# Kernel optimization log

Measured on AMD Instinct MI355X. Metric: run time of the kernel, lower is better.

## Reference

```python
import jax, jax.numpy as jnp
import numpy as np

D_MODEL = 1024
NHEAD = 16
HEAD_DIM = D_MODEL // NHEAD
ROPE_BASE = 10000.0


def rope_cos_sin(seq_len, dim, dtype=jnp.float32):
    inv_freq = 1.0 / (ROPE_BASE ** (jnp.arange(0, dim, 2, dtype=jnp.float32) / dim))
    t = jnp.arange(seq_len, dtype=jnp.float32)
    freqs = jnp.einsum('i,j->ij', t, inv_freq)        # [S, dim/2]
    emb = jnp.concatenate([freqs, freqs], axis=-1)    # [S, dim]
    return emb.astype(dtype), jnp.cos(emb).astype(dtype), jnp.sin(emb).astype(dtype)


def rotate_half(x):
    x1, x2 = jnp.split(x, 2, axis=-1)
    return jnp.concatenate([-x2, x1], axis=-1)


def setup_inputs() -> dict:
    key = jax.random.key(0)
    ks = jax.random.split(key, 11)
    B, S, D = 2, 2048, D_MODEL
    std = 1.0 / np.sqrt(D)
    return {
        'query': jax.random.normal(ks[0], (B, S, D), jnp.float32),
        'key_': jax.random.normal(ks[1], (B, S, D), jnp.float32),
        'value': jax.random.normal(ks[2], (B, S, D), jnp.float32),
        'Wq': jax.random.uniform(ks[3], (D, D), jnp.float32, -std, std),
        'bq': jax.random.uniform(ks[4], (D,), jnp.float32, -std, std),
        'Wk': jax.random.uniform(ks[5], (D, D), jnp.float32, -std, std),
        'bk': jax.random.uniform(ks[6], (D,), jnp.float32, -std, std),
        'Wv': jax.random.uniform(ks[7], (D, D), jnp.float32, -std, std),
        'bv': jax.random.uniform(ks[8], (D,), jnp.float32, -std, std),
        'Wo': jax.random.uniform(ks[9], (D, D), jnp.float32, -std, std),
        'bo': jax.random.uniform(ks[10], (D,), jnp.float32, -std, std),
    }


def reference(query, key_, value, Wq, bq, Wk, bk, Wv, bv, Wo, bo):
    B, T, D = query.shape
    S = key_.shape[1]
    H, Hd = NHEAD, HEAD_DIM
    scale = Hd ** -0.5
    # projections (torch Linear: x @ W^T + b), reshape to [B, H, L, Hd]
    q = (query @ Wq.T + bq).reshape(B, T, H, Hd).transpose(0, 2, 1, 3)
    k = (key_ @ Wk.T + bk).reshape(B, S, H, Hd).transpose(0, 2, 1, 3)
    v = (value @ Wv.T + bv).reshape(B, S, H, Hd).transpose(0, 2, 1, 3)
    # RoPE
    _, cos, sin = rope_cos_sin(max(T, S), Hd, query.dtype)
    cos_q, sin_q = cos[:T][None, None], sin[:S][None, None]
    q = q * cos_q + rotate_half(q) * sin_q
    k = k * cos_q + rotate_half(k) * sin_q
    # attention
    scores = jnp.einsum('bhtd,bhsd->bhts', q, k) * scale
    attn = jax.nn.softmax(scores, axis=-1)
    out = jnp.einsum('bhts,bhsd->bhtd', attn, v)
    out = out.transpose(0, 2, 1, 3).reshape(B, T, D)
    return out @ Wo.T + bo
```

## Files before the change

### kernel.cpp

```cpp
#include <hip/hip_runtime.h>
#include <hip/hip_bf16.h>
#include <math.h>

using bf16x8 = __attribute__((ext_vector_type(8))) short;
using f32x4  = __attribute__((ext_vector_type(4))) float;

#define MFMA16(a,b,c) __builtin_amdgcn_mfma_f32_16x16x32_bf16(a,b,c,0,0,0)

static __device__ __forceinline__ short f2bf(float f) {
    __hip_bfloat16 h = __float2bfloat16(f);
    return *reinterpret_cast<short*>(&h);
}

__global__ void prep_cast(const float* q, const float* k, const float* v,
                          const float* wq, const float* wk, const float* wv, const float* wo,
                          short* xq, short* xk, short* xv,
                          short* bwq, short* bwk, short* bwv, short* bwo) {
    const long NBIG = 1L << 20;
    const long NW   = 1L << 18;
    const long total = 3*NBIG + 4*NW;
    for (long i = (long)blockIdx.x*blockDim.x + threadIdx.x; i < total; i += (long)gridDim.x*blockDim.x) {
        const float* src; short* dst; long j = i;
        if (j < NBIG)              { src = q;  dst = xq;  }
        else if ((j -= NBIG) < NBIG) { src = k;  dst = xk;  }
        else if ((j -= NBIG) < NBIG) { src = v;  dst = xv;  }
        else if ((j -= NBIG) < NW)   { src = wq; dst = bwq; }
        else if ((j -= NW) < NW)     { src = wk; dst = bwk; }
        else if ((j -= NW) < NW)     { src = wv; dst = bwv; }
        else { j -= NW;              src = wo; dst = bwo; }
        float4 f = reinterpret_cast<const float4*>(src)[j];
        ushort4 o;
        o.x = (ushort)f2bf(f.x); o.y = (ushort)f2bf(f.y);
        o.z = (ushort)f2bf(f.z); o.w = (ushort)f2bf(f.w);
        reinterpret_cast<ushort4*>(dst)[j] = o;
    }
}

__global__ void rope_table(float* cost, float* sint) {
    int i = blockIdx.x*blockDim.x + threadIdx.x;
    int s = i >> 5, j = i & 31;
    double inv = pow(10000.0, -(double)j / 32.0);
    double a = (double)s * inv;
    cost[i] = (float)cos(a);
    sint[i] = (float)sin(a);
}

__device__ __forceinline__ void gemm_tile(const short* A, const short* B,
                                          int brow, int bcol, f32x4 (&acc)[4][4]) {
    __shared__ __align__(16) short Al[128*32];
    __shared__ __align__(16) short Bl[128*32];
    const int t = threadIdx.x;
    const int l = t & 63, qi = l & 15, h = l >> 4;
    const int w = t >> 6, wr = w >> 1, wc = w & 1;
    const f32x4 z4 = {0.f, 0.f, 0.f, 0.f};
#pragma unroll
    for (int i = 0; i < 4; ++i)
#pragma unroll
        for (int j = 0; j < 4; ++j) acc[i][j] = z4;

    for (int kt = 0; kt < 32; ++kt) {
        __syncthreads();
#pragma unroll
        for (int cc = 0; cc < 2; ++cc) {
            int c = t + (cc << 8);
            int row = c >> 2, off = (c & 3) << 3;
            int4 va = *(const int4*)(A + (long)(brow + row)*1024 + (kt << 5) + off);
            int4 vb = *(const int4*)(B + (long)(bcol + row)*1024 + (kt << 5) + off);
            *(int4*)(Al + (c << 3)) = va;
            *(int4*)(Bl + (c << 3)) = vb;
        }
        __syncthreads();
        bf16x8 af[4], bfr[4];
#pragma unroll
        for (int mf = 0; mf < 4; ++mf)
            af[mf] = *(const bf16x8*)(Al + (wr*64 + mf*16 + qi)*32 + h*8);
#pragma unroll
        for (int nf = 0; nf < 4; ++nf)
            bfr[nf] = *(const bf16x8*)(Bl + (wc*64 + nf*16 + qi)*32 + h*8);
#pragma unroll
        for (int mf = 0; mf < 4; ++mf)
#pragma unroll
            for (int nf = 0; nf < 4; ++nf)
                acc[mf][nf] = MFMA16(af[mf], bfr[nf], acc[mf][nf]);
    }
}

__global__ __launch_bounds__(256, 2)
void gemm_qkv_kernel(const short* xq, const short* xk, const short* xv,
                     const short* wq, const short* wk, const short* wv,
                     const float* biq, const float* bik, const float* biv,
                     short* qo, short* ko, short* vo,
                     const float* cost, const float* sint) {
    const int mode = blockIdx.z;
    const short* A    = mode == 0 ? xq  : (mode == 1 ? xk  : xv);
    const short* B    = mode == 0 ? wq  : (mode == 1 ? wk  : wv);
    const float* bias = mode == 0 ? biq : (mode == 1 ? bik : biv);
    const int brow = blockIdx.x * 128, bcol = blockIdx.y * 128;
    f32x4 acc[4][4];
    gemm_tile(A, B, brow, bcol, acc);

    const int t = threadIdx.x;
    const int l = t & 63, qi = l & 15, h = l >> 4;
    const int w = t >> 6, wr = w >> 1, wc = w & 1;
    const int n0 = bcol + wc*64, m0 = brow + wr*64;

    if (mode < 2) {
        short* dst = mode == 0 ? qo : ko;
        const float sc = (mode == 0) ? 0.125f : 1.0f;
#pragma unroll
        for (int nf = 0; nf < 2; ++nf) {
            const int j = nf*16 + qi;
            const float b0 = bias[n0 + nf*16 + qi];
            const float b1 = bias[n0 + (nf+2)*16 + qi];
#pragma unroll
            for (int mf = 0; mf < 4; ++mf) {
#pragma unroll
                for (int r = 0; r < 4; ++r) {
                    int m = m0 + mf*16 + 4*h + r;
                    int s = m & 2047;
                    float c  = cost[s*32 + j];
                    float si = sint[s*32 + j];
                    float x0 = acc[mf][nf  ][r] + b0;
                    float x1 = acc[mf][nf+2][r] + b1;
                    dst[(long)m*1024 + n0 + nf*16 + qi]      = f2bf((x0*c - x1*si) * sc);
                    dst[(long)m*1024 + n0 + (nf+2)*16 + qi]  = f2bf((x1*c + x0*si) * sc);
                }
            }
        }
    } else {
#pragma unroll
        for (int mf = 0; mf < 4; ++mf) {
#pragma unroll
            for (int nf = 0; nf < 4; ++nf) {
                int col = n0 + nf*16 + qi;
                float bb = bias[col];
                int mbase = m0 + mf*16 + 4*h;
                int bb_  = mbase >> 11, s0 = mbase & 2047;
                int hh = col >> 6, d = col & 63;
                ushort4 pk;
                pk.x = (ushort)f2bf(acc[mf][nf][0] + bb);
                pk.y = (ushort)f2bf(acc[mf][nf][1] + bb);
                pk.z = (ushort)f2bf(acc[mf][nf][2] + bb);
                pk.w = (ushort)f2bf(acc[mf][nf][3] + bb);
                *(ushort4*)(vo + (long)((bb_*16 + hh)*64 + d)*2048 + s0) = pk;
            }
        }
    }
}

__global__ __launch_bounds__(256, 2)
void gemm_o_kernel(const short* A, const short* B, const float* bias, float* out) {
    const int brow = blockIdx.x * 128, bcol = blockIdx.y * 128;
    f32x4 acc[4][4];
    gemm_tile(A, B, brow, bcol, acc);
    const int t = threadIdx.x;
    const int l = t & 63, qi = l & 15, h = l >> 4;
    const int w = t >> 6, wr = w >> 1, wc = w & 1;
    const int n0 = bcol + wc*64, m0 = brow + wr*64;
#pragma unroll
    for (int nf = 0; nf < 4; ++nf) {
        float bb = bias[n0 + nf*16 + qi];
#pragma unroll
        for (int mf = 0; mf < 4; ++mf) {
#pragma unroll
            for (int r = 0; r < 4; ++r) {
                int m = m0 + mf*16 + 4*h + r;
                out[(long)m*1024 + n0 + nf*16 + qi] = acc[mf][nf][r] + bb;
            }
        }
    }
}

__global__ __launch_bounds__(256, 2)
void attn_kernel(const short* qw, const short* kw, const short* vtw, short* ow) {
    __shared__ __align__(16) short Kl[64*64];
    __shared__ __align__(16) short Vl[64*64];
    __shared__ __align__(16) short Pl[4][32*64];
    const int t = threadIdx.x;
    const int w = t >> 6, l = t & 63, qi = l & 15, h = l >> 4;
    const int b = blockIdx.z, hh = blockIdx.y;
    const long qrow0 = (long)b*2048 + blockIdx.x*128 + w*32;
    short* myP = &Pl[w][0];

    bf16x8 bqf[2][2];
#pragma unroll
    for (int nf = 0; nf < 2; ++nf)
#pragma unroll
        for (int kf = 0; kf < 2; ++kf)
            bqf[nf][kf] = *(const bf16x8*)(qw + (qrow0 + nf*16 + qi)*1024 + hh*64 + kf*32 + h*8);

    const f32x4 z4 = {0.f, 0.f, 0.f, 0.f};
    f32x4 o[2][4];
#pragma unroll
    for (int mi = 0; mi < 2; ++mi)
#pragma unroll
        for (int nd = 0; nd < 4; ++nd) o[mi][nd] = z4;
    float mrun[2] = {-INFINITY, -INFINITY};
    float lrun[2] = {0.f, 0.f};

    const short* Kg = kw  + (long)b*2048*1024 + hh*64;
    const short* Vg = vtw + (long)(b*16 + hh)*64*2048;

    for (int jt = 0; jt < 32; ++jt) {
        __syncthreads();
#pragma unroll
        for (int cc = 0; cc < 2; ++cc) {
            int c  = t + (cc << 8);
            int r0 = c >> 3, e0 = (c & 7) << 3;
            int4 kv = *(const int4*)(Kg + (long)(jt*64 + r0)*1024 + e0);
            int4 vv = *(const int4*)(Vg + (long)r0*2048 + jt*64 + e0);
            *(int4*)((char*)Kl + (((r0*64 + e0)*2) ^ ((r0 & 7) << 4))) = kv;
            *(int4*)((char*)Vl + (((r0*64 + e0)*2) ^ ((r0 & 7) << 4))) = vv;
        }
        __syncthreads();

        f32x4 sc[4][2];
#pragma unroll
        for (int mf = 0; mf < 4; ++mf) { sc[mf][0] = z4; sc[mf][1] = z4; }
#pragma unroll
        for (int kf = 0; kf < 2; ++kf) {
#pragma unroll
            for (int mf = 0; mf < 4; ++mf) {
                bf16x8 ka = *(const bf16x8*)((char*)Kl +
                    ((((mf*16 + qi)*64 + kf*32 + h*8)*2) ^ ((qi & 7) << 4)));
                sc[mf][0] = MFMA16(ka, bqf[0][kf], sc[mf][0]);
                sc[mf][1] = MFMA16(ka, bqf[1][kf], sc[mf][1]);
            }
        }

        float csc[2];
#pragma unroll
        for (int nf = 0; nf < 2; ++nf) {
            float tm = -INFINITY;
#pragma unroll
            for (int mf = 0; mf < 4; ++mf)
#pragma unroll
                for (int r = 0; r < 4; ++r) tm = fmaxf(tm, sc[mf][nf][r]);
            tm = fmaxf(tm, __shfl_xor(tm, 16));
            tm = fmaxf(tm, __shfl_xor(tm, 32));
            float mnew = fmaxf(mrun[nf], tm);
            float corr = __expf(mrun[nf] - mnew);
            float ts = 0.f;
#pragma unroll
            for (int mf = 0; mf < 4; ++mf) {
                float p0 = __expf(sc[mf][nf][0] - mnew);
                float p1 = __expf(sc[mf][nf][1] - mnew);
                float p2 = __expf(sc[mf][nf][2] - mnew);
                float p3 = __expf(sc[mf][nf][3] - mnew);
                ts += p0 + p1 + p2 + p3;
                ushort4 pk;
                pk.x = (ushort)f2bf(p0); pk.y = (ushort)f2bf(p1);
                pk.z = (ushort)f2bf(p2); pk.w = (ushort)f2bf(p3);
                *(ushort4*)((char*)myP +
                    ((((nf*16 + qi)*64 + mf*16 + 4*h)*2) ^ ((qi & 7) << 4))) = pk;
            }
            ts += __shfl_xor(ts, 16);
            ts += __shfl_xor(ts, 32);
            lrun[nf] = lrun[nf]*corr + ts;
            mrun[nf] = mnew;
            csc[nf] = corr;
        }

#pragma unroll
        for (int mi = 0; mi < 2; ++mi)
#pragma unroll
            for (int r = 0; r < 4; ++r) {
                float f = __shfl(csc[mi], 4*h + r);
#pragma unroll
                for (int nd = 0; nd < 4; ++nd) o[mi][nd][r] *= f;
            }

#pragma unroll
        for (int kf = 0; kf < 2; ++kf) {
            bf16x8 pa[2], vb[4];
#pragma unroll
            for (int mi = 0; mi < 2; ++mi)
                pa[mi] = *(const bf16x8*)((char*)myP +
                    ((((mi*16 + qi)*64 + kf*32 + h*8)*2) ^ ((qi & 7) << 4)));
#pragma unroll
            for (int nd = 0; nd < 4; ++nd)
                vb[nd] = *(const bf16x8*)((char*)Vl +
                    ((((nd*16 + qi)*64 + kf*32 + h*8)*2) ^ ((qi & 7) << 4)));
#pragma unroll
            for (int mi = 0; mi < 2; ++mi)
#pragma unroll
                for (int nd = 0; nd < 4; ++nd)
                    o[mi][nd] = MFMA16(pa[mi], vb[nd], o[mi][nd]);
        }
    }

    float rinv[2] = {1.f/lrun[0], 1.f/lrun[1]};
#pragma unroll
    for (int mi = 0; mi < 2; ++mi)
#pragma unroll
        for (int r = 0; r < 4; ++r) {
            float f = __shfl(rinv[mi], 4*h + r);
#pragma unroll
            for (int nd = 0; nd < 4; ++nd)
                ow[(qrow0 + mi*16 + 4*h + r)*1024 + hh*64 + nd*16 + qi] =
                    f2bf(o[mi][nd][r] * f);
        }
}

extern "C" void kernel_launch(void* const* d_in, const int* in_sizes, int n_in,
                              void* d_out, int out_size, void* d_ws, size_t ws_size,
                              hipStream_t stream) {
    const float* query = (const float*)d_in[0];
    const float* key_  = (const float*)d_in[1];
    const float* value = (const float*)d_in[2];
    const float* Wq = (const float*)d_in[3];
    const float* bq = (const float*)d_in[4];
    const float* Wk = (const float*)d_in[5];
    const float* bk = (const float*)d_in[6];
    const float* Wv = (const float*)d_in[7];
    const float* bv = (const float*)d_in[8];
    const float* Wo = (const float*)d_in[9];
    const float* bo = (const float*)d_in[10];
    float* out = (float*)d_out;

    char* ws = (char*)d_ws;
    const size_t MB = 1u << 20;
    short* xq  = (short*)(ws);
    short* xk  = (short*)(ws + 8*MB);
    short* xv  = (short*)(ws + 16*MB);
    short* wqb = (short*)(ws + 24*MB);
    short* wkb = (short*)(ws + 26*MB);
    short* wvb = (short*)(ws + 28*MB);
    short* wob = (short*)(ws + 30*MB);
    short* qws = (short*)(ws + 32*MB);
    short* kws = (short*)(ws + 40*MB);
    short* vtw = (short*)(ws + 48*MB);
    float* cost = (float*)(ws + 56*MB);
    float* sint = (float*)(ws + 56*MB + 2048*32*4);
    short* attn = xq;

    hipLaunchKernelGGL(prep_cast, dim3(2048), dim3(256), 0, stream,
                       query, key_, value, Wq, Wk, Wv, Wo,
                       xq, xk, xv, wqb, wkb, wvb, wob);
    hipLaunchKernelGGL(rope_table, dim3(256), dim3(256), 0, stream, cost, sint);
    hipLaunchKernelGGL(gemm_qkv_kernel, dim3(32, 8, 3), dim3(256), 0, stream,
                       xq, xk, xv, wqb, wkb, wvb, bq, bk, bv,
                       qws, kws, vtw, cost, sint);
    hipLaunchKernelGGL(attn_kernel, dim3(16, 16, 2), dim3(256), 0, stream,
                       qws, kws, vtw, attn);
    hipLaunchKernelGGL(gemm_o_kernel, dim3(32, 8), dim3(256), 0, stream,
                       attn, wob, bo, out);
}
```

Before: 250.5 us.

## Double-buffer K/V tiles in attention and use direct global-to-LDS loads in GEMM

The attention kernel now double-buffers its K/V shared-memory tiles. It issues the global loads for the next tile into registers before the current tile's MFMAs, writes them to the other buffer afterward, and drops one barrier per iteration. It also raises wave priority around the MFMA blocks with s_setprio. The GEMM tile loader switches to the global_load_lds builtin, so data goes straight from global memory into LDS without a register round trip. The double buffer doubles K/V LDS use, which may affect occupancy at two blocks per CU, and the direct-to-LDS path relies on the per-wave layout matching the fragment reads.

Result: slower. 268.2 us (+7.0%).

```diff
diff --git a/kernel.cpp b/kernel.cpp
--- a/kernel.cpp
+++ b/kernel.cpp
@@ -6,6 +6,10 @@
 using f32x4  = __attribute__((ext_vector_type(4))) float;
 
 #define MFMA16(a,b,c) __builtin_amdgcn_mfma_f32_16x16x32_bf16(a,b,c,0,0,0)
+
+#define GLOAD_LDS16(g, s) __builtin_amdgcn_global_load_lds( \
+    (const __attribute__((address_space(1))) unsigned int*)(const void*)(g), \
+    (__attribute__((address_space(3))) unsigned int*)(void*)(s), 16, 0, 0)
 
 static __device__ __forceinline__ short f2bf(float f) {
     __hip_bfloat16 h = __float2bfloat16(f);
@@ -58,17 +62,19 @@
 #pragma unroll
         for (int j = 0; j < 4; ++j) acc[i][j] = z4;
 
+    const int srow = w*32 + (l >> 2);
+    const int scol = (l & 3) << 3;
+    const short* ga = A + (long)(brow + srow)*1024 + scol;
+    const short* gb = B + (long)(bcol + srow)*1024 + scol;
+    short* la = Al + w*32*32;
+    short* lb = Bl + w*32*32;
+
     for (int kt = 0; kt < 32; ++kt) {
         __syncthreads();
-#pragma unroll
-        for (int cc = 0; cc < 2; ++cc) {
-            int c = t + (cc << 8);
-            int row = c >> 2, off = (c & 3) << 3;
-            int4 va = *(const int4*)(A + (long)(brow + row)*1024 + (kt << 5) + off);
-            int4 vb = *(const int4*)(B + (long)(bcol + row)*1024 + (kt << 5) + off);
-            *(int4*)(Al + (c << 3)) = va;
-            *(int4*)(Bl + (c << 3)) = vb;
-        }
+        GLOAD_LDS16(ga + (kt << 5),            la);
+        GLOAD_LDS16(ga + (kt << 5) + 16*1024,  la + 16*32);
+        GLOAD_LDS16(gb + (kt << 5),            lb);
+        GLOAD_LDS16(gb + (kt << 5) + 16*1024,  lb + 16*32);
         __syncthreads();
         bf16x8 af[4], bfr[4];
 #pragma unroll
@@ -173,8 +179,8 @@
 
 __global__ __launch_bounds__(256, 2)
 void attn_kernel(const short* qw, const short* kw, const short* vtw, short* ow) {
-    __shared__ __align__(16) short Kl[64*64];
-    __shared__ __align__(16) short Vl[64*64];
+    __shared__ __align__(16) short Kl[2][64*64];
+    __shared__ __align__(16) short Vl[2][64*64];
     __shared__ __align__(16) short Pl[4][32*64];
     const int t = threadIdx.x;
     const int w = t >> 6, l = t & 63, qi = l & 15, h = l >> 4;
@@ -201,32 +207,47 @@
     const short* Kg = kw  + (long)b*2048*1024 + hh*64;
     const short* Vg = vtw + (long)(b*16 + hh)*64*2048;
 
+    const int c0 = t, c1 = t + 256;
+    const int r0a = c0 >> 3, e0a = (c0 & 7) << 3;
+    const int r0b = c1 >> 3, e0b = (c1 & 7) << 3;
+    int4 kreg[2], vreg[2];
+
+    kreg[0] = *(const int4*)(Kg + (long)r0a*1024 + e0a);
+    vreg[0] = *(const int4*)(Vg + (long)r0a*2048 + e0a);
+    kreg[1] = *(const int4*)(Kg + (long)r0b*1024 + e0b);
+    vreg[1] = *(const int4*)(Vg + (long)r0b*2048 + e0b);
+    *(int4*)((char*)Kl[0] + (((r0a*64 + e0a)*2) ^ ((r0a & 7) << 4))) = kreg[0];
+    *(int4*)((char*)Vl[0] + (((r0a*64 + e0a)*2) ^ ((r0a & 7) << 4))) = vreg[0];
+    *(int4*)((char*)Kl[1 & 0] + (((r0b*64 + e0b)*2) ^ ((r0b & 7) << 4))) = kreg[1];
+    *(int4*)((char*)Vl[0] + (((r0b*64 + e0b)*2) ^ ((r0b & 7) << 4))) = vreg[1];
+
+    int cur = 0;
     for (int jt = 0; jt < 32; ++jt) {
         __syncthreads();
-#pragma unroll
-        for (int cc = 0; cc < 2; ++cc) {
-            int c  = t + (cc << 8);
-            int r0 = c >> 3, e0 = (c & 7) << 3;
-            int4 kv = *(const int4*)(Kg + (long)(jt*64 + r0)*1024 + e0);
-            int4 vv = *(const int4*)(Vg + (long)r0*2048 + jt*64 + e0);
-            *(int4*)((char*)Kl + (((r0*64 + e0)*2) ^ ((r0 & 7) << 4))) = kv;
-            *(int4*)((char*)Vl + (((r0*64 + e0)*2) ^ ((r0 & 7) << 4))) = vv;
-        }
-        __syncthreads();
+        if (jt < 31) {
+            kreg[0] = *(const int4*)(Kg + (long)((jt+1)*64 + r0a)*1024 + e0a);
+            vreg[0] = *(const int4*)(Vg + (long)r0a*2048 + (jt+1)*64 + e0a);
+            kreg[1] = *(const int4*)(Kg + (long)((jt+1)*64 + r0b)*1024 + e0b);
+            vreg[1] = *(const int4*)(Vg + (long)r0b*2048 + (jt+1)*64 + e0b);
+        }
+        const short* Kc = Kl[cur];
+        const short* Vc = Vl[cur];
 
         f32x4 sc[4][2];
 #pragma unroll
         for (int mf = 0; mf < 4; ++mf) { sc[mf][0] = z4; sc[mf][1] = z4; }
+        __builtin_amdgcn_s_setprio(1);
 #pragma unroll
         for (int kf = 0; kf < 2; ++kf) {
 #pragma unroll
             for (int mf = 0; mf < 4; ++mf) {
-                bf16x8 ka = *(const bf16x8*)((char*)Kl +
+                bf16x8 ka = *(const bf16x8*)((const char*)Kc +
                     ((((mf*16 + qi)*64 + kf*32 + h*8)*2) ^ ((qi & 7) << 4)));
                 sc[mf][0] = MFMA16(ka, bqf[0][kf], sc[mf][0]);
                 sc[mf][1] = MFMA16(ka, bqf[1][kf], sc[mf][1]);
             }
         }
+        __builtin_amdgcn_s_setprio(0);
 
         float csc[2];
 #pragma unroll
@@ -270,6 +291,7 @@
                 for (int nd = 0; nd < 4; ++nd) o[mi][nd][r] *= f;
             }
 
+        __builtin_amdgcn_s_setprio(1);
 #pragma unroll
         for (int kf = 0; kf < 2; ++kf) {
             bf16x8 pa[2], vb[4];
@@ -279,7 +301,7 @@
                     ((((mi*16 + qi)*64 + kf*32 + h*8)*2) ^ ((qi & 7) << 4)));
 #pragma unroll
             for (int nd = 0; nd < 4; ++nd)
-                vb[nd] = *(const bf16x8*)((char*)Vl +
+                vb[nd] = *(const bf16x8*)((const char*)Vc +
                     ((((nd*16 + qi)*64 + kf*32 + h*8)*2) ^ ((qi & 7) << 4)));
 #pragma unroll
             for (int mi = 0; mi < 2; ++mi)
@@ -287,6 +309,16 @@
                 for (int nd = 0; nd < 4; ++nd)
                     o[mi][nd] = MFMA16(pa[mi], vb[nd], o[mi][nd]);
         }
+        __builtin_amdgcn_s_setprio(0);
+
+        if (jt < 31) {
+            int nb = cur ^ 1;
+            *(int4*)((char*)Kl[nb] + (((r0a*64 + e0a)*2) ^ ((r0a & 7) << 4))) = kreg[0];
+            *(int4*)((char*)Vl[nb] + (((r0a*64 + e0a)*2) ^ ((r0a & 7) << 4))) = vreg[0];
+            *(int4*)((char*)Kl[nb] + (((r0b*64 + e0b)*2) ^ ((r0b & 7) << 4))) = kreg[1];
+            *(int4*)((char*)Vl[nb] + (((r0b*64 + e0b)*2) ^ ((r0b & 7) << 4))) = vreg[1];
+        }
+        cur ^= 1;
     }
 
     float rinv[2] = {1.f/lrun[0], 1.f/lrun[1]};
```

## Double-buffer GEMM tiles with direct global-to-LDS loads and MFMA priority hints

Applied to the files above, without the earlier changes.

The shared GEMM tile loop now uses two LDS buffers filled by global_load_lds, so the next K-slice streams into shared memory while MFMAs run on the current one, with one barrier per iteration instead of two. The GEMM kernels' launch bounds go from 2 to 3 blocks per CU. s_setprio brackets are added around the MFMA sections in both the GEMMs and the attention kernel. Shared memory per GEMM block doubles, which may limit the higher occupancy target, and the tighter launch bound may force register spills.

Result: no change. 246.3 us (-1.7%).

```diff
diff --git a/kernel.cpp b/kernel.cpp
--- a/kernel.cpp
+++ b/kernel.cpp
@@ -6,6 +6,10 @@
 using f32x4  = __attribute__((ext_vector_type(4))) float;
 
 #define MFMA16(a,b,c) __builtin_amdgcn_mfma_f32_16x16x32_bf16(a,b,c,0,0,0)
+
+#define GLOAD_LDS16(g, s) __builtin_amdgcn_global_load_lds( \
+    (const __attribute__((address_space(1))) unsigned int*)(const void*)(g), \
+    (__attribute__((address_space(3))) unsigned int*)(void*)(s), 16, 0, 0)
 
 static __device__ __forceinline__ short f2bf(float f) {
     __hip_bfloat16 h = __float2bfloat16(f);
@@ -47,8 +51,8 @@
 
 __device__ __forceinline__ void gemm_tile(const short* A, const short* B,
                                           int brow, int bcol, f32x4 (&acc)[4][4]) {
-    __shared__ __align__(16) short Al[128*32];
-    __shared__ __align__(16) short Bl[128*32];
+    __shared__ __align__(16) short Al[2][128*32];
+    __shared__ __align__(16) short Bl[2][128*32];
     const int t = threadIdx.x;
     const int l = t & 63, qi = l & 15, h = l >> 4;
     const int w = t >> 6, wr = w >> 1, wc = w & 1;
@@ -58,34 +62,49 @@
 #pragma unroll
         for (int j = 0; j < 4; ++j) acc[i][j] = z4;
 
+    const int srow = w*32 + (l >> 2);
+    const int scol = (l & 3) << 3;
+    const short* ga = A + (long)(brow + srow)*1024 + scol;
+    const short* gb = B + (long)(bcol + srow)*1024 + scol;
+    const int lo = w*32*32;
+
+    GLOAD_LDS16(ga,            Al[0] + lo);
+    GLOAD_LDS16(ga + 16*1024,  Al[0] + lo + 16*32);
+    GLOAD_LDS16(gb,            Bl[0] + lo);
+    GLOAD_LDS16(gb + 16*1024,  Bl[0] + lo + 16*32);
+    asm volatile("s_waitcnt vmcnt(0)");
+    __syncthreads();
+
+    int cur = 0;
     for (int kt = 0; kt < 32; ++kt) {
-        __syncthreads();
-#pragma unroll
-        for (int cc = 0; cc < 2; ++cc) {
-            int c = t + (cc << 8);
-            int row = c >> 2, off = (c & 3) << 3;
-            int4 va = *(const int4*)(A + (long)(brow + row)*1024 + (kt << 5) + off);
-            int4 vb = *(const int4*)(B + (long)(bcol + row)*1024 + (kt << 5) + off);
-            *(int4*)(Al + (c << 3)) = va;
-            *(int4*)(Bl + (c << 3)) = vb;
-        }
-        __syncthreads();
+        if (kt < 31) {
+            int nb = cur ^ 1;
+            GLOAD_LDS16(ga + ((kt+1) << 5),            Al[nb] + lo);
+            GLOAD_LDS16(ga + ((kt+1) << 5) + 16*1024,  Al[nb] + lo + 16*32);
+            GLOAD_LDS16(gb + ((kt+1) << 5),            Bl[nb] + lo);
+            GLOAD_LDS16(gb + ((kt+1) << 5) + 16*1024,  Bl[nb] + lo + 16*32);
+        }
         bf16x8 af[4], bfr[4];
 #pragma unroll
         for (int mf = 0; mf < 4; ++mf)
-            af[mf] = *(const bf16x8*)(Al + (wr*64 + mf*16 + qi)*32 + h*8);
+            af[mf] = *(const bf16x8*)(Al[cur] + (wr*64 + mf*16 + qi)*32 + h*8);
 #pragma unroll
         for (int nf = 0; nf < 4; ++nf)
-            bfr[nf] = *(const bf16x8*)(Bl + (wc*64 + nf*16 + qi)*32 + h*8);
+            bfr[nf] = *(const bf16x8*)(Bl[cur] + (wc*64 + nf*16 + qi)*32 + h*8);
+        __builtin_amdgcn_s_setprio(1);
 #pragma unroll
         for (int mf = 0; mf < 4; ++mf)
 #pragma unroll
             for (int nf = 0; nf < 4; ++nf)
                 acc[mf][nf] = MFMA16(af[mf], bfr[nf], acc[mf][nf]);
-    }
-}
-
-__global__ __launch_bounds__(256, 2)
+        __builtin_amdgcn_s_setprio(0);
+        asm volatile("s_waitcnt vmcnt(0)");
+        __syncthreads();
+        cur ^= 1;
+    }
+}
+
+__global__ __launch_bounds__(256, 3)
 void gemm_qkv_kernel(const short* xq, const short* xk, const short* xv,
                      const short* wq, const short* wk, const short* wv,
                      const float* biq, const float* bik, const float* biv,
@@ -148,7 +167,7 @@
     }
 }
 
-__global__ __launch_bounds__(256, 2)
+__global__ __launch_bounds__(256, 3)
 void gemm_o_kernel(const short* A, const short* B, const float* bias, float* out) {
     const int brow = blockIdx.x * 128, bcol = blockIdx.y * 128;
     f32x4 acc[4][4];
@@ -217,6 +236,7 @@
         f32x4 sc[4][2];
 #pragma unroll
         for (int mf = 0; mf < 4; ++mf) { sc[mf][0] = z4; sc[mf][1] = z4; }
+        __builtin_amdgcn_s_setprio(1);
 #pragma unroll
         for (int kf = 0; kf < 2; ++kf) {
 #pragma unroll
@@ -227,6 +247,7 @@
                 sc[mf][1] = MFMA16(ka, bqf[1][kf], sc[mf][1]);
             }
         }
+        __builtin_amdgcn_s_setprio(0);
 
         float csc[2];
 #pragma unroll
@@ -270,6 +291,7 @@
                 for (int nd = 0; nd < 4; ++nd) o[mi][nd][r] *= f;
             }
 
+        __builtin_amdgcn_s_setprio(1);
 #pragma unroll
         for (int kf = 0; kf < 2; ++kf) {
             bf16x8 pa[2], vb[4];
@@ -287,6 +309,7 @@
                 for (int nd = 0; nd < 4; ++nd)
                     o[mi][nd] = MFMA16(pa[mi], vb[nd], o[mi][nd]);
         }
+        __builtin_amdgcn_s_setprio(0);
     }
 
     float rinv[2] = {1.f/lrun[0], 1.f/lrun[1]};
```
